# Kernel tuning notes

Hardware: AMD Instinct MI355X
Metric: run time of the kernel (lower is better)

Reference implementation:

```python
import jax, jax.numpy as jnp
import numpy as np

# ---- static configuration (from init_kwargs) ----
K = 2                 # kernel_size -> (2K+1)^2 = 25 window offsets
WIN = 2 * K + 1       # 5
A = WIN * WIN         # 25 window slots (ir_in replicated A times)
MUL_IN = 16           # multiplicity of each input irrep (16x0e + 16x1e)
MUL_OUT = 32          # 32x0e + 32x1e
SH0 = float(1.0 / (2.0 * np.sqrt(np.pi)))       # Y_l=0, e3nn 'integral' norm
SH1 = float(np.sqrt(3.0 / (4.0 * np.pi)))       # Y_l=1 scale (normalize=False)
CG_110 = float(1.0 / np.sqrt(3.0))              # CG for 1x1 -> 0 (dot/sqrt3)
CG_111 = float(1.0 / np.sqrt(2.0))              # CG for 1x1 -> 1 (cross/sqrt2)
# path normalization: out irrep gets 1/sqrt(fan_in) with fan = n_paths * mul_u
A0 = float(1.0 / np.sqrt(2 * A * MUL_IN))       # 0e fed by paths (0e,0e)+(1e,1e) per slot
A1 = float(1.0 / np.sqrt(3 * A * MUL_IN))       # 1e fed by (0e,1e)+(1e,0e)+(1e,1e)


def setup_inputs() -> dict:
    key = jax.random.key(0)
    ks = jax.random.split(key, 7)
    feat = jax.random.normal(ks[0], (8, 64, 64, 64), dtype=jnp.float32)
    spin = jax.random.normal(ks[1], (8, 64, 64, 3), dtype=jnp.float32)
    wshape = (A, MUL_IN, MUL_OUT)  # one uvw block per window slot per path type
    W_000 = jax.random.normal(ks[2], wshape, dtype=jnp.float32)
    W_110 = jax.random.normal(ks[3], wshape, dtype=jnp.float32)
    W_011 = jax.random.normal(ks[4], wshape, dtype=jnp.float32)
    W_101 = jax.random.normal(ks[5], wshape, dtype=jnp.float32)
    W_111 = jax.random.normal(ks[6], wshape, dtype=jnp.float32)
    return {"feat": feat, "spin": spin, "W_000": W_000, "W_110": W_110,
            "W_011": W_011, "W_101": W_101, "W_111": W_111}


def spin2colsq2d(feat):
    # circular im2col: (N,Lx,Ly,F) -> (N,Lx,Ly,A,F)
    N, Lx, Ly, F = feat.shape
    p = jnp.pad(feat, ((0, 0), (K, K), (K, K), (0, 0)), mode='wrap')
    cols = [p[:, ix:ix + Lx, iy:iy + Ly, :]
            for ix in range(WIN) for iy in range(WIN)]
    return jnp.stack(cols, axis=3)


def reference(feat, spin, W_000, W_110, W_011, W_101, W_111):
    col = spin2colsq2d(feat)                                  # (N,Lx,Ly,A,64)
    x0 = col[..., :MUL_IN]                                    # (N,Lx,Ly,A,16) scalars
    x1 = col[..., MUL_IN:].reshape(col.shape[:-1] + (MUL_IN, 3))  # (N,Lx,Ly,A,16,3)
    # spherical harmonics of spin, l=0..1, normalize=False, integral norm
    sh1 = SH1 * spin                                          # (N,Lx,Ly,3)
    # ---- paths into 0e output ----
    dot = jnp.einsum('nxyaui,nxyi->nxyau', x1, sh1) * CG_110  # 1e x 1e -> 0e
    out0 = A0 * (SH0 * jnp.einsum('nxyau,auw->nxyw', x0, W_000)
                 + jnp.einsum('nxyau,auw->nxyw', dot, W_110))  # (N,Lx,Ly,32)
    # ---- paths into 1e output ----
    cross = jnp.cross(x1, sh1[..., None, None, :]) * CG_111   # 1e x 1e -> 1e
    out1 = A1 * (jnp.einsum('nxyau,nxyi,auw->nxywi', x0, sh1, W_011)
                 + SH0 * jnp.einsum('nxyaui,auw->nxywi', x1, W_101)
                 + jnp.einsum('nxyaui,auw->nxywi', cross, W_111))  # (N,Lx,Ly,32,3)
    out1 = out1.reshape(out1.shape[:-2] + (MUL_OUT * 3,))
    return jnp.concatenate([out0, out1], axis=-1)             # (N,Lx,Ly,128)
```

## Files before the change

kernel.cpp:

```cpp
#include <hip/hip_runtime.h>


typedef __attribute__((ext_vector_type(8))) short short8;
typedef __attribute__((ext_vector_type(16))) float f32x16;
typedef __attribute__((ext_vector_type(4))) float float4v;

typedef __attribute__((address_space(3))) unsigned char lds_u8_t;
typedef const __attribute__((address_space(1))) unsigned char g_u8_t;

#define FEATT_BYTES (8u * 64u * 64u * 64u * 2u)
#define BT_OFFSET   FEATT_BYTES

#define MFMA32(A, B, C) __builtin_amdgcn_mfma_f32_32x32x16_bf16(A, B, C, 0, 0, 0)

__device__ __forceinline__ unsigned short f2bf(float f) {
    unsigned int u = __float_as_uint(f);
    return (unsigned short)((u + 0x7FFFu + ((u >> 16) & 1u)) >> 16);
}

__global__ __launch_bounds__(256) void prep_kernel(
    const float* __restrict__ feat,
    const float* __restrict__ W000, const float* __restrict__ W110,
    const float* __restrict__ W011, const float* __restrict__ W101,
    const float* __restrict__ W111,
    unsigned char* __restrict__ ws)
{
    int tid = threadIdx.x;
    int b = blockIdx.x;
    if (b < 512) {
        __shared__ float sf[64][68];
        size_t base = (size_t)b * 4096;
        #pragma unroll
        for (int i = 0; i < 4; ++i) {
            int e = tid + i * 256;
            float4v v = *(const float4v*)(feat + base + (size_t)e * 4);
            int px = e >> 4;
            int c  = (e & 15) * 4;
            sf[px][c + 0] = v[0]; sf[px][c + 1] = v[1];
            sf[px][c + 2] = v[2]; sf[px][c + 3] = v[3];
        }
        __syncthreads();
        unsigned short* dst = (unsigned short*)ws + base;
        #pragma unroll
        for (int i = 0; i < 2; ++i) {
            int t = tid + i * 256;
            int s = t >> 6, px = t & 63;
            short8 o;
            #pragma unroll
            for (int j = 0; j < 8; ++j) {
                int chp = s * 8 + j;
                int c = (chp < 16) ? chp : (16 + 3 * ((chp - 16) & 15) + ((chp - 16) >> 4));
                o[j] = (short)f2bf(sf[px][c]);
            }
            *(short8*)(dst + s * 512 + px * 8) = o;
        }
    } else {
        int t = (b - 512) * 256 + tid;
        if (t >= 4000) return;
        int a = t / 160, colv = t - a * 160;
        int arr = colv >> 5, w = colv & 31;
        const float* Wp = (arr == 0) ? W000 : (arr == 1) ? W011
                        : (arr == 2) ? W110 : (arr == 3) ? W101 : W111;
        unsigned short tmp[16];
        #pragma unroll
        for (int k = 0; k < 16; ++k) tmp[k] = f2bf(Wp[a * 512 + k * 32 + w]);
        unsigned short* d = (unsigned short*)(ws + BT_OFFSET) + (size_t)t * 16;
        *(short8*)(d)     = *(short8*)(tmp);
        *(short8*)(d + 8) = *(short8*)(tmp + 8);
    }
}

__global__ __launch_bounds__(256, 4) void spinconv_mfma_kernel(
    const unsigned char* __restrict__ featT8,
    const unsigned char* __restrict__ bt,
    const float* __restrict__ spin,
    float* __restrict__ out)
{
    const float SH0f   = 0.28209479177387814f;
    const float CG110f = 0.5773502691896258f;
    const float CG111f = 0.7071067811865476f;
    const float A0f    = 0.035355339059327376f;
    const float A1f    = 0.028867513459481287f;

    __shared__ __align__(16) unsigned char fl[1440 * 16];
    __shared__ float s_lds[96];

    int tid = threadIdx.x;
    int b = blockIdx.x;
    int L = ((b & 7) << 7) + (b >> 3);
    int column = L >> 1;
    int x = column & 63;
    int y0 = (L & 1) << 5;

    int lane = tid & 63;
    int wv4 = tid >> 6;

    #pragma unroll
    for (int i = 0; i < 6; ++i) {
        int e = tid + (i << 8);
        int g = e / 36;
        int l = e - g * 36;
        int dx = g >> 3, slot = g & 7;
        int X = (x + dx + 62) & 63;
        int y = (y0 + l + 62) & 63;
        const unsigned char* src = featT8
            + (size_t)(column - x + X) * 8192 + slot * 1024 + y * 16;
        if (e < 1440)
            __builtin_amdgcn_global_load_lds((g_u8_t*)src,
                (lds_u8_t*)(fl + ((i << 8) + (tid & ~63)) * 16), 16, 0, 0);
    }
    if (tid < 96) {
        s_lds[tid] = 0.4886025119029199f
                   * spin[((size_t)column * 64 + y0) * 3 + tid];
    }
    __syncthreads();

    int role = (wv4 + (b & 3)) & 3;
    int col = lane & 31;
    int khalf = lane >> 5;

    const unsigned char* bbase = bt + col * 32 + khalf * 16;
    float* rowbuf = (float*)fl;

    f32x16 zz;
    #pragma unroll
    for (int i = 0; i < 16; ++i) zz[i] = 0.f;

    f32x16 ac0 = zz, ac1 = zz, ac2 = zz;

    if (role == 0) {
        short8 B0c, B1c, B0n, B1n, Axc, Axn;
        auto loadB = [&](int a, short8& b0, short8& b1) {
            const unsigned char* p = bbase + a * 5120;
            b0 = *(const short8*)(p);
            b1 = *(const short8*)(p + 1024);
        };
        auto loadA = [&](int a, short8& ax) {
            int ix = a / 5;
            int iy = a - ix * 5;
            ax = *(const short8*)(fl + ix * 4608 + khalf * 576 + (col + iy) * 16);
        };
        loadB(0, B0c, B1c);
        loadA(0, Axc);
        #pragma unroll
        for (int ap = 0; ap < 25; ap += 2) {
            if (ap + 1 < 25) { loadB(ap + 1, B0n, B1n); loadA(ap + 1, Axn); }
            __builtin_amdgcn_s_setprio(1);
            ac0 = MFMA32(Axc, B0c, ac0);
            ac1 = MFMA32(Axc, B1c, ac1);
            __builtin_amdgcn_s_setprio(0);
            if (ap + 1 < 25) {
                if (ap + 2 < 25) { loadB(ap + 2, B0c, B1c); loadA(ap + 2, Axc); }
                __builtin_amdgcn_s_setprio(1);
                ac0 = MFMA32(Axn, B0n, ac0);
                ac1 = MFMA32(Axn, B1n, ac1);
                __builtin_amdgcn_s_setprio(0);
            }
        }
    } else {
        const int matoff = (role + 1) << 10;
        short8 Bc, Bn, C0c, C1c, C2c, C0n, C1n, C2n;
        auto loadB = [&](int a, short8& bb) {
            bb = *(const short8*)(bbase + a * 5120 + matoff);
        };
        auto loadA = [&](int a, short8& c0, short8& c1, short8& c2) {
            int ix = a / 5;
            int iy = a - ix * 5;
            const unsigned char* ab = fl + ix * 4608 + (col + iy) * 16;
            c0 = *(const short8*)(ab + (2 + khalf) * 576);
            c1 = *(const short8*)(ab + (4 + khalf) * 576);
            c2 = *(const short8*)(ab + (6 + khalf) * 576);
        };
        loadB(0, Bc);
        loadA(0, C0c, C1c, C2c);
        #pragma unroll
        for (int ap = 0; ap < 25; ap += 2) {
            if (ap + 1 < 25) { loadB(ap + 1, Bn); loadA(ap + 1, C0n, C1n, C2n); }
            __builtin_amdgcn_s_setprio(1);
            ac0 = MFMA32(C0c, Bc, ac0);
            ac1 = MFMA32(C1c, Bc, ac1);
            ac2 = MFMA32(C2c, Bc, ac2);
            __builtin_amdgcn_s_setprio(0);
            if (ap + 1 < 25) {
                if (ap + 2 < 25) { loadB(ap + 2, Bc); loadA(ap + 2, C0c, C1c, C2c); }
                __builtin_amdgcn_s_setprio(1);
                ac0 = MFMA32(C0n, Bn, ac0);
                ac1 = MFMA32(C1n, Bn, ac1);
                ac2 = MFMA32(C2n, Bn, ac2);
                __builtin_amdgcn_s_setprio(0);
            }
        }
    }

    __syncthreads();

    {
        if (role == 0) {
            #pragma unroll
            for (int r = 0; r < 16; ++r) {
                int yl = (r & 3) + ((r >> 2) << 3) + (khalf << 2);
                float s0 = s_lds[yl * 3 + 0];
                float s1 = s_lds[yl * 3 + 1];
                float s2 = s_lds[yl * 3 + 2];
                float S000 = ac0[r], S011 = ac1[r];
                float* rb = rowbuf + yl * 128;
                float* rp = rb + 32 + 3 * col;
                rb[col] = A0f * SH0f * S000;
                rp[0] = A1f * s0 * S011;
                rp[1] = A1f * s1 * S011;
                rp[2] = A1f * s2 * S011;
            }
        }
        __syncthreads();
        if (role == 1) {
            #pragma unroll
            for (int r = 0; r < 16; ++r) {
                int yl = (r & 3) + ((r >> 2) << 3) + (khalf << 2);
                float s0 = s_lds[yl * 3 + 0];
                float s1 = s_lds[yl * 3 + 1];
                float s2 = s_lds[yl * 3 + 2];
                rowbuf[yl * 128 + col] +=
                    A0f * CG110f * (s0 * ac0[r] + s1 * ac1[r] + s2 * ac2[r]);
            }
        } else if (role == 2) {
            #pragma unroll
            for (int r = 0; r < 16; ++r) {
                int yl = (r & 3) + ((r >> 2) << 3) + (khalf << 2);
                float* rp = rowbuf + yl * 128 + 32 + 3 * col;
                rp[0] += A1f * SH0f * ac0[r];
                rp[1] += A1f * SH0f * ac1[r];
                rp[2] += A1f * SH0f * ac2[r];
            }
        }
        __syncthreads();
        if (role == 3) {
            #pragma unroll
            for (int r = 0; r < 16; ++r) {
                int yl = (r & 3) + ((r >> 2) << 3) + (khalf << 2);
                float s0 = s_lds[yl * 3 + 0];
                float s1 = s_lds[yl * 3 + 1];
                float s2 = s_lds[yl * 3 + 2];
                float U0 = ac0[r], U1 = ac1[r], U2 = ac2[r];
                float* rp = rowbuf + yl * 128 + 32 + 3 * col;
                rp[0] += A1f * CG111f * (U1 * s2 - U2 * s1);
                rp[1] += A1f * CG111f * (U2 * s0 - U0 * s2);
                rp[2] += A1f * CG111f * (U0 * s1 - U1 * s0);
            }
        }
        __syncthreads();
    }

    float* ob = out + ((size_t)column * 64 + y0) * 128;
    #pragma unroll
    for (int i = 0; i < 4; ++i) {
        int e = (tid + (i << 8)) << 2;
        *(float4v*)(ob + e) = *(const float4v*)(rowbuf + e);
    }
}

extern "C" void kernel_launch(void* const* d_in, const int* in_sizes, int n_in,
                              void* d_out, int out_size, void* d_ws, size_t ws_size,
                              hipStream_t stream) {
    const float* feat = (const float*)d_in[0];
    const float* spin = (const float*)d_in[1];
    const float* W000 = (const float*)d_in[2];
    const float* W110 = (const float*)d_in[3];
    const float* W011 = (const float*)d_in[4];
    const float* W101 = (const float*)d_in[5];
    const float* W111 = (const float*)d_in[6];
    float* out = (float*)d_out;
    unsigned char* ws = (unsigned char*)d_ws;

    hipLaunchKernelGGL(prep_kernel, dim3(528), dim3(256), 0, stream,
                       feat, W000, W110, W011, W101, W111, ws);
    hipLaunchKernelGGL(spinconv_mfma_kernel, dim3(1024), dim3(256), 0, stream,
                       ws, ws + BT_OFFSET, spin, out);
}
```

Baseline: 24.60 us.

## Process two half-columns per block with double-buffered LDS prefetch

Each block now handles a full 64-row column as two 32-row halves. It issues the global-to-LDS loads for both halves up front and waits only on the first half (vmcnt(5)) before starting the first half's MFMAs, so the second half's load overlaps compute. The grid is halved to 512 blocks, LDS use roughly doubles, and the occupancy hint drops from 4 to 3 blocks per CU. The cost is fewer resident blocks and reliance on a hand-set waitcnt matching exactly how many loads each thread issued.

```diff
diff --git a/kernel.cpp b/kernel.cpp
--- a/kernel.cpp
+++ b/kernel.cpp
@@ -70,7 +70,7 @@
     }
 }
 
-__global__ __launch_bounds__(256, 4) void spinconv_mfma_kernel(
+__global__ __launch_bounds__(256, 3) void spinconv_mfma_kernel(
     const unsigned char* __restrict__ featT8,
     const unsigned char* __restrict__ bt,
     const float* __restrict__ spin,
@@ -82,126 +82,134 @@
     const float A0f    = 0.035355339059327376f;
     const float A1f    = 0.028867513459481287f;
 
-    __shared__ __align__(16) unsigned char fl[1440 * 16];
-    __shared__ float s_lds[96];
+    __shared__ __align__(16) unsigned char fl[2][23040];
+    __shared__ float s_lds[192];
 
     int tid = threadIdx.x;
     int b = blockIdx.x;
-    int L = ((b & 7) << 7) + (b >> 3);
-    int column = L >> 1;
+    int column = ((b & 7) << 6) + (b >> 3);
     int x = column & 63;
-    int y0 = (L & 1) << 5;
+    int colbase = column - x;
 
     int lane = tid & 63;
     int wv4 = tid >> 6;
 
+    float spinval = 0.f;
+    if (tid < 192) spinval = 0.4886025119029199f * spin[(size_t)column * 192 + tid];
+
     #pragma unroll
-    for (int i = 0; i < 6; ++i) {
-        int e = tid + (i << 8);
-        int g = e / 36;
-        int l = e - g * 36;
-        int dx = g >> 3, slot = g & 7;
-        int X = (x + dx + 62) & 63;
-        int y = (y0 + l + 62) & 63;
-        const unsigned char* src = featT8
-            + (size_t)(column - x + X) * 8192 + slot * 1024 + y * 16;
-        if (e < 1440)
-            __builtin_amdgcn_global_load_lds((g_u8_t*)src,
-                (lds_u8_t*)(fl + ((i << 8) + (tid & ~63)) * 16), 16, 0, 0);
+    for (int th = 0; th < 2; ++th) {
+        #pragma unroll
+        for (int i = 0; i < 6; ++i) {
+            int e = tid + (i << 8);
+            if (e < 1440) {
+                int g = e / 36;
+                int l = e - g * 36;
+                int dx = g >> 3, slot = g & 7;
+                int X = (x + dx + 62) & 63;
+                int y = ((th << 5) + l + 62) & 63;
+                const unsigned char* src = featT8
+                    + (size_t)(colbase + X) * 8192 + slot * 1024 + y * 16;
+                __builtin_amdgcn_global_load_lds((g_u8_t*)src,
+                    (lds_u8_t*)(fl[th] + ((i << 8) + (tid & ~63)) * 16), 16, 0, 0);
+            }
+        }
     }
-    if (tid < 96) {
-        s_lds[tid] = 0.4886025119029199f
-                   * spin[((size_t)column * 64 + y0) * 3 + tid];
-    }
-    __syncthreads();
+    asm volatile("s_waitcnt vmcnt(5)" ::: "memory");
+    __builtin_amdgcn_sched_barrier(0);
+    __builtin_amdgcn_s_barrier();
 
     int role = (wv4 + (b & 3)) & 3;
     int col = lane & 31;
     int khalf = lane >> 5;
-
     const unsigned char* bbase = bt + col * 32 + khalf * 16;
-    float* rowbuf = (float*)fl;
 
     f32x16 zz;
     #pragma unroll
     for (int i = 0; i < 16; ++i) zz[i] = 0.f;
 
-    f32x16 ac0 = zz, ac1 = zz, ac2 = zz;
-
-    if (role == 0) {
-        short8 B0c, B1c, B0n, B1n, Axc, Axn;
-        auto loadB = [&](int a, short8& b0, short8& b1) {
-            const unsigned char* p = bbase + a * 5120;
-            b0 = *(const short8*)(p);
-            b1 = *(const short8*)(p + 1024);
-        };
-        auto loadA = [&](int a, short8& ax) {
-            int ix = a / 5;
-            int iy = a - ix * 5;
-            ax = *(const short8*)(fl + ix * 4608 + khalf * 576 + (col + iy) * 16);
-        };
-        loadB(0, B0c, B1c);
-        loadA(0, Axc);
-        #pragma unroll
-        for (int ap = 0; ap < 25; ap += 2) {
-            if (ap + 1 < 25) { loadB(ap + 1, B0n, B1n); loadA(ap + 1, Axn); }
-            __builtin_amdgcn_s_setprio(1);
-            ac0 = MFMA32(Axc, B0c, ac0);
-            ac1 = MFMA32(Axc, B1c, ac1);
-            __builtin_amdgcn_s_setprio(0);
-            if (ap + 1 < 25) {
-                if (ap + 2 < 25) { loadB(ap + 2, B0c, B1c); loadA(ap + 2, Axc); }
+    #pragma unroll
+    for (int th = 0; th < 2; ++th) {
+        const unsigned char* ft = fl[th];
+        f32x16 ac0 = zz, ac1 = zz, ac2 = zz;
+
+        if (role == 0) {
+            short8 B0c, B1c, B0n, B1n, Axc, Axn;
+            auto loadB = [&](int a, short8& b0, short8& b1) {
+                const unsigned char* p = bbase + a * 5120;
+                b0 = *(const short8*)(p);
+                b1 = *(const short8*)(p + 1024);
+            };
+            auto loadA = [&](int a, short8& ax) {
+                int ix = a / 5;
+                int iy = a - ix * 5;
+                ax = *(const short8*)(ft + ix * 4608 + khalf * 576 + (col + iy) * 16);
+            };
+            loadB(0, B0c, B1c);
+            loadA(0, Axc);
+            #pragma unroll
+            for (int ap = 0; ap < 25; ap += 2) {
+                if (ap + 1 < 25) { loadB(ap + 1, B0n, B1n); loadA(ap + 1, Axn); }
                 __builtin_amdgcn_s_setprio(1);
-                ac0 = MFMA32(Axn, B0n, ac0);
-                ac1 = MFMA32(Axn, B1n, ac1);
+                ac0 = MFMA32(Axc, B0c, ac0);
+                ac1 = MFMA32(Axc, B1c, ac1);
                 __builtin_amdgcn_s_setprio(0);
-            }
-        }
-    } else {
-        const int matoff = (role + 1) << 10;
-        short8 Bc, Bn, C0c, C1c, C2c, C0n, C1n, C2n;
-        auto loadB = [&](int a, short8& bb) {
-            bb = *(const short8*)(bbase + a * 5120 + matoff);
-        };
-        auto loadA = [&](int a, short8& c0, short8& c1, short8& c2) {
-            int ix = a / 5;
-            int iy = a - ix * 5;
-            const unsigned char* ab = fl + ix * 4608 + (col + iy) * 16;
-            c0 = *(const short8*)(ab + (2 + khalf) * 576);
-            c1 = *(const short8*)(ab + (4 + khalf) * 576);
-            c2 = *(const short8*)(ab + (6 + khalf) * 576);
-        };
-        loadB(0, Bc);
-        loadA(0, C0c, C1c, C2c);
-        #pragma unroll
-        for (int ap = 0; ap < 25; ap += 2) {
-            if (ap + 1 < 25) { loadB(ap + 1, Bn); loadA(ap + 1, C0n, C1n, C2n); }
-            __builtin_amdgcn_s_setprio(1);
-            ac0 = MFMA32(C0c, Bc, ac0);
-            ac1 = MFMA32(C1c, Bc, ac1);
-            ac2 = MFMA32(C2c, Bc, ac2);
-            __builtin_amdgcn_s_setprio(0);
-            if (ap + 1 < 25) {
-                if (ap + 2 < 25) { loadB(ap + 2, Bc); loadA(ap + 2, C0c, C1c, C2c); }
+                if (ap + 1 < 25) {
+                    if (ap + 2 < 25) { loadB(ap + 2, B0c, B1c); loadA(ap + 2, Axc); }
+                    __builtin_amdgcn_s_setprio(1);
+                    ac0 = MFMA32(Axn, B0n, ac0);
+                    ac1 = MFMA32(Axn, B1n, ac1);
+                    __builtin_amdgcn_s_setprio(0);
+                }
+            }
+        } else {
+            const int matoff = (role + 1) << 10;
+            short8 Bc, Bn, C0c, C1c, C2c, C0n, C1n, C2n;
+            auto loadB = [&](int a, short8& bb) {
+                bb = *(const short8*)(bbase + a * 5120 + matoff);
+            };
+            auto loadA = [&](int a, short8& c0, short8& c1, short8& c2) {
+                int ix = a / 5;
+                int iy = a - ix * 5;
+                const unsigned char* ab = ft + ix * 4608 + (col + iy) * 16;
+                c0 = *(const short8*)(ab + (2 + khalf) * 576);
+                c1 = *(const short8*)(ab + (4 + khalf) * 576);
+                c2 = *(const short8*)(ab + (6 + khalf) * 576);
+            };
+            loadB(0, Bc);
+            loadA(0, C0c, C1c, C2c);
+            #pragma unroll
+            for (int ap = 0; ap < 25; ap += 2) {
+                if (ap + 1 < 25) { loadB(ap + 1, Bn); loadA(ap + 1, C0n, C1n, C2n); }
                 __builtin_amdgcn_s_setprio(1);
-                ac0 = MFMA32(C0n, Bn, ac0);
-                ac1 = MFMA32(C1n, Bn, ac1);
-                ac2 = MFMA32(C2n, Bn, ac2);
+                ac0 = MFMA32(C0c, Bc, ac0);
+                ac1 = MFMA32(C1c, Bc, ac1);
+                ac2 = MFMA32(C2c, Bc, ac2);
                 __builtin_amdgcn_s_setprio(0);
-            }
-        }
-    }
-
-    __syncthreads();
-
-    {
+                if (ap + 1 < 25) {
+                    if (ap + 2 < 25) { loadB(ap + 2, Bc); loadA(ap + 2, C0c, C1c, C2c); }
+                    __builtin_amdgcn_s_setprio(1);
+                    ac0 = MFMA32(C0n, Bn, ac0);
+                    ac1 = MFMA32(C1n, Bn, ac1);
+                    ac2 = MFMA32(C2n, Bn, ac2);
+                    __builtin_amdgcn_s_setprio(0);
+                }
+            }
+        }
+
+        if (th == 0 && tid < 192) s_lds[tid] = spinval;
+        __syncthreads();
+
+        float* rowbuf = (float*)fl[th];
+        const float* sp = s_lds + th * 96;
+
         if (role == 0) {
             #pragma unroll
             for (int r = 0; r < 16; ++r) {
                 int yl = (r & 3) + ((r >> 2) << 3) + (khalf << 2);
-                float s0 = s_lds[yl * 3 + 0];
-                float s1 = s_lds[yl * 3 + 1];
-                float s2 = s_lds[yl * 3 + 2];
+                float s0 = sp[yl * 3 + 0];
+                float s1 = sp[yl * 3 + 1];
+                float s2 = sp[yl * 3 + 2];
                 float S000 = ac0[r], S011 = ac1[r];
                 float* rb = rowbuf + yl * 128;
                 float* rp = rb + 32 + 3 * col;
@@ -216,9 +224,9 @@
             #pragma unroll
             for (int r = 0; r < 16; ++r) {
                 int yl = (r & 3) + ((r >> 2) << 3) + (khalf << 2);
-                float s0 = s_lds[yl * 3 + 0];
-                float s1 = s_lds[yl * 3 + 1];
-                float s2 = s_lds[yl * 3 + 2];
+                float s0 = sp[yl * 3 + 0];
+                float s1 = sp[yl * 3 + 1];
+                float s2 = sp[yl * 3 + 2];
                 rowbuf[yl * 128 + col] +=
                     A0f * CG110f * (s0 * ac0[r] + s1 * ac1[r] + s2 * ac2[r]);
             }
@@ -237,9 +245,9 @@
             #pragma unroll
             for (int r = 0; r < 16; ++r) {
                 int yl = (r & 3) + ((r >> 2) << 3) + (khalf << 2);
-                float s0 = s_lds[yl * 3 + 0];
-                float s1 = s_lds[yl * 3 + 1];
-                float s2 = s_lds[yl * 3 + 2];
+                float s0 = sp[yl * 3 + 0];
+                float s1 = sp[yl * 3 + 1];
+                float s2 = sp[yl * 3 + 2];
                 float U0 = ac0[r], U1 = ac1[r], U2 = ac2[r];
                 float* rp = rowbuf + yl * 128 + 32 + 3 * col;
                 rp[0] += A1f * CG111f * (U1 * s2 - U2 * s1);
@@ -248,13 +256,13 @@
             }
         }
         __syncthreads();
-    }
-
-    float* ob = out + ((size_t)column * 64 + y0) * 128;
-    #pragma unroll
-    for (int i = 0; i < 4; ++i) {
-        int e = (tid + (i << 8)) << 2;
-        *(float4v*)(ob + e) = *(const float4v*)(rowbuf + e);
+
+        float* ob = out + ((size_t)column * 64 + (th << 5)) * 128;
+        #pragma unroll
+        for (int i = 0; i < 4; ++i) {
+            int e = (tid + (i << 8)) << 2;
+            *(float4v*)(ob + e) = *(const float4v*)(rowbuf + e);
+        }
     }
 }
 
@@ -273,6 +281,6 @@
 
     hipLaunchKernelGGL(prep_kernel, dim3(528), dim3(256), 0, stream,
                        feat, W000, W110, W011, W101, W111, ws);
-    hipLaunchKernelGGL(spinconv_mfma_kernel, dim3(1024), dim3(256), 0, stream,
+    hipLaunchKernelGGL(spinconv_mfma_kernel, dim3(512), dim3(256), 0, stream,
                        ws, ws + BT_OFFSET, spin, out);
 }
```

New measurement: 26.65 us. 8.3% more time.

## Split work across two waves per block and write outputs directly from registers

Applied to the files above, without the earlier changes.

Reduces the block from four waves to two. Wave 0 computes the 0e-output paths plus the scalar-to-vector path, and wave 1 computes the W101 and W111 vector paths with six accumulators. The LDS rowbuf staging and its multiple barrier-separated accumulate phases are replaced by a small LDS exchange of one accumulator, followed by direct global stores of the combined results. This removes the serialized epilogue and most barriers. In exchange each wave issues more MFMAs and holds more live registers, so there are fewer waves per block to hide latency, and the scattered 12-byte stores are less coalesced.

```diff
diff --git a/kernel.cpp b/kernel.cpp
--- a/kernel.cpp
+++ b/kernel.cpp
@@ -12,6 +12,8 @@
 #define BT_OFFSET   FEATT_BYTES
 
 #define MFMA32(A, B, C) __builtin_amdgcn_mfma_f32_32x32x16_bf16(A, B, C, 0, 0, 0)
+
+struct F3 { float a, b, c; };
 
 __device__ __forceinline__ unsigned short f2bf(float f) {
     unsigned int u = __float_as_uint(f);
@@ -70,7 +72,7 @@
     }
 }
 
-__global__ __launch_bounds__(256, 4) void spinconv_mfma_kernel(
+__global__ __launch_bounds__(128, 3) void spinconv_mfma_kernel(
     const unsigned char* __restrict__ featT8,
     const unsigned char* __restrict__ bt,
     const float* __restrict__ spin,
@@ -83,6 +85,7 @@
     const float A1f    = 0.028867513459481287f;
 
     __shared__ __align__(16) unsigned char fl[1440 * 16];
+    __shared__ float sbuf[16][64];
     __shared__ float s_lds[96];
 
     int tid = threadIdx.x;
@@ -93,21 +96,22 @@
     int y0 = (L & 1) << 5;
 
     int lane = tid & 63;
-    int wv4 = tid >> 6;
+    int wv = tid >> 6;
 
     #pragma unroll
-    for (int i = 0; i < 6; ++i) {
-        int e = tid + (i << 8);
-        int g = e / 36;
-        int l = e - g * 36;
-        int dx = g >> 3, slot = g & 7;
-        int X = (x + dx + 62) & 63;
-        int y = (y0 + l + 62) & 63;
-        const unsigned char* src = featT8
-            + (size_t)(column - x + X) * 8192 + slot * 1024 + y * 16;
-        if (e < 1440)
+    for (int i = 0; i < 12; ++i) {
+        int e = tid + (i << 7);
+        if (e < 1440) {
+            int g = e / 36;
+            int l = e - g * 36;
+            int dx = g >> 3, slot = g & 7;
+            int X = (x + dx + 62) & 63;
+            int y = (y0 + l + 62) & 63;
+            const unsigned char* src = featT8
+                + (size_t)(column - x + X) * 8192 + slot * 1024 + y * 16;
             __builtin_amdgcn_global_load_lds((g_u8_t*)src,
-                (lds_u8_t*)(fl + ((i << 8) + (tid & ~63)) * 16), 16, 0, 0);
+                (lds_u8_t*)(fl + ((i << 7) + (tid & ~63)) * 16), 16, 0, 0);
+        }
     }
     if (tid < 96) {
         s_lds[tid] = 0.4886025119029199f
@@ -115,53 +119,67 @@
     }
     __syncthreads();
 
-    int role = (wv4 + (b & 3)) & 3;
+    int role = wv ^ (b & 1);
     int col = lane & 31;
     int khalf = lane >> 5;
-
     const unsigned char* bbase = bt + col * 32 + khalf * 16;
-    float* rowbuf = (float*)fl;
 
     f32x16 zz;
     #pragma unroll
     for (int i = 0; i < 16; ++i) zz[i] = 0.f;
 
-    f32x16 ac0 = zz, ac1 = zz, ac2 = zz;
+    f32x16 ac0 = zz, ac1 = zz, ac2 = zz, ac3 = zz, ac4 = zz, ac5 = zz;
 
     if (role == 0) {
-        short8 B0c, B1c, B0n, B1n, Axc, Axn;
-        auto loadB = [&](int a, short8& b0, short8& b1) {
+        short8 B0c, B1c, B2c, B0n, B1n, B2n;
+        short8 Axc, C0c, C1c, C2c, Axn, C0n, C1n, C2n;
+        auto loadB = [&](int a, short8& b0, short8& b1, short8& b2) {
             const unsigned char* p = bbase + a * 5120;
             b0 = *(const short8*)(p);
             b1 = *(const short8*)(p + 1024);
-        };
-        auto loadA = [&](int a, short8& ax) {
+            b2 = *(const short8*)(p + 2048);
+        };
+        auto loadA = [&](int a, short8& ax, short8& c0, short8& c1, short8& c2) {
             int ix = a / 5;
             int iy = a - ix * 5;
-            ax = *(const short8*)(fl + ix * 4608 + khalf * 576 + (col + iy) * 16);
-        };
-        loadB(0, B0c, B1c);
-        loadA(0, Axc);
+            const unsigned char* ab = fl + ix * 4608 + (col + iy) * 16;
+            ax = *(const short8*)(ab + khalf * 576);
+            c0 = *(const short8*)(ab + (2 + khalf) * 576);
+            c1 = *(const short8*)(ab + (4 + khalf) * 576);
+            c2 = *(const short8*)(ab + (6 + khalf) * 576);
+        };
+        loadB(0, B0c, B1c, B2c);
+        loadA(0, Axc, C0c, C1c, C2c);
         #pragma unroll
         for (int ap = 0; ap < 25; ap += 2) {
-            if (ap + 1 < 25) { loadB(ap + 1, B0n, B1n); loadA(ap + 1, Axn); }
+            if (ap + 1 < 25) { loadB(ap + 1, B0n, B1n, B2n); loadA(ap + 1, Axn, C0n, C1n, C2n); }
             __builtin_amdgcn_s_setprio(1);
             ac0 = MFMA32(Axc, B0c, ac0);
             ac1 = MFMA32(Axc, B1c, ac1);
+            ac2 = MFMA32(C0c, B2c, ac2);
+            ac3 = MFMA32(C1c, B2c, ac3);
+            ac4 = MFMA32(C2c, B2c, ac4);
             __builtin_amdgcn_s_setprio(0);
             if (ap + 1 < 25) {
-                if (ap + 2 < 25) { loadB(ap + 2, B0c, B1c); loadA(ap + 2, Axc); }
+                if (ap + 2 < 25) { loadB(ap + 2, B0c, B1c, B2c); loadA(ap + 2, Axc, C0c, C1c, C2c); }
                 __builtin_amdgcn_s_setprio(1);
                 ac0 = MFMA32(Axn, B0n, ac0);
                 ac1 = MFMA32(Axn, B1n, ac1);
+                ac2 = MFMA32(C0n, B2n, ac2);
+                ac3 = MFMA32(C1n, B2n, ac3);
+                ac4 = MFMA32(C2n, B2n, ac4);
                 __builtin_amdgcn_s_setprio(0);
             }
         }
+        #pragma unroll
+        for (int r = 0; r < 16; ++r) sbuf[r][lane] = ac1[r];
     } else {
-        const int matoff = (role + 1) << 10;
-        short8 Bc, Bn, C0c, C1c, C2c, C0n, C1n, C2n;
-        auto loadB = [&](int a, short8& bb) {
-            bb = *(const short8*)(bbase + a * 5120 + matoff);
+        short8 B3c, B4c, B3n, B4n;
+        short8 C0c, C1c, C2c, C0n, C1n, C2n;
+        auto loadB = [&](int a, short8& b3, short8& b4) {
+            const unsigned char* p = bbase + a * 5120;
+            b3 = *(const short8*)(p + 3072);
+            b4 = *(const short8*)(p + 4096);
         };
         auto loadA = [&](int a, short8& c0, short8& c1, short8& c2) {
             int ix = a / 5;
@@ -171,22 +189,28 @@
             c1 = *(const short8*)(ab + (4 + khalf) * 576);
             c2 = *(const short8*)(ab + (6 + khalf) * 576);
         };
-        loadB(0, Bc);
+        loadB(0, B3c, B4c);
         loadA(0, C0c, C1c, C2c);
         #pragma unroll
         for (int ap = 0; ap < 25; ap += 2) {
-            if (ap + 1 < 25) { loadB(ap + 1, Bn); loadA(ap + 1, C0n, C1n, C2n); }
+            if (ap + 1 < 25) { loadB(ap + 1, B3n, B4n); loadA(ap + 1, C0n, C1n, C2n); }
             __builtin_amdgcn_s_setprio(1);
-            ac0 = MFMA32(C0c, Bc, ac0);
-            ac1 = MFMA32(C1c, Bc, ac1);
-            ac2 = MFMA32(C2c, Bc, ac2);
+            ac0 = MFMA32(C0c, B3c, ac0);
+            ac3 = MFMA32(C0c, B4c, ac3);
+            ac1 = MFMA32(C1c, B3c, ac1);
+            ac4 = MFMA32(C1c, B4c, ac4);
+            ac2 = MFMA32(C2c, B3c, ac2);
+            ac5 = MFMA32(C2c, B4c, ac5);
             __builtin_amdgcn_s_setprio(0);
             if (ap + 1 < 25) {
-                if (ap + 2 < 25) { loadB(ap + 2, Bc); loadA(ap + 2, C0c, C1c, C2c); }
+                if (ap + 2 < 25) { loadB(ap + 2, B3c, B4c); loadA(ap + 2, C0c, C1c, C2c); }
                 __builtin_amdgcn_s_setprio(1);
-                ac0 = MFMA32(C0n, Bn, ac0);
-                ac1 = MFMA32(C1n, Bn, ac1);
-                ac2 = MFMA32(C2n, Bn, ac2);
+                ac0 = MFMA32(C0n, B3n, ac0);
+                ac3 = MFMA32(C0n, B4n, ac3);
+                ac1 = MFMA32(C1n, B3n, ac1);
+                ac4 = MFMA32(C1n, B4n, ac4);
+                ac2 = MFMA32(C2n, B3n, ac2);
+                ac5 = MFMA32(C2n, B4n, ac5);
                 __builtin_amdgcn_s_setprio(0);
             }
         }
@@ -194,67 +218,34 @@
 
     __syncthreads();
 
-    {
-        if (role == 0) {
-            #pragma unroll
-            for (int r = 0; r < 16; ++r) {
-                int yl = (r & 3) + ((r >> 2) << 3) + (khalf << 2);
-                float s0 = s_lds[yl * 3 + 0];
-                float s1 = s_lds[yl * 3 + 1];
-                float s2 = s_lds[yl * 3 + 2];
-                float S000 = ac0[r], S011 = ac1[r];
-                float* rb = rowbuf + yl * 128;
-                float* rp = rb + 32 + 3 * col;
-                rb[col] = A0f * SH0f * S000;
-                rp[0] = A1f * s0 * S011;
-                rp[1] = A1f * s1 * S011;
-                rp[2] = A1f * s2 * S011;
-            }
-        }
-        __syncthreads();
-        if (role == 1) {
-            #pragma unroll
-            for (int r = 0; r < 16; ++r) {
-                int yl = (r & 3) + ((r >> 2) << 3) + (khalf << 2);
-                float s0 = s_lds[yl * 3 + 0];
-                float s1 = s_lds[yl * 3 + 1];
-                float s2 = s_lds[yl * 3 + 2];
-                rowbuf[yl * 128 + col] +=
-                    A0f * CG110f * (s0 * ac0[r] + s1 * ac1[r] + s2 * ac2[r]);
-            }
-        } else if (role == 2) {
-            #pragma unroll
-            for (int r = 0; r < 16; ++r) {
-                int yl = (r & 3) + ((r >> 2) << 3) + (khalf << 2);
-                float* rp = rowbuf + yl * 128 + 32 + 3 * col;
-                rp[0] += A1f * SH0f * ac0[r];
-                rp[1] += A1f * SH0f * ac1[r];
-                rp[2] += A1f * SH0f * ac2[r];
-            }
-        }
-        __syncthreads();
-        if (role == 3) {
-            #pragma unroll
-            for (int r = 0; r < 16; ++r) {
-                int yl = (r & 3) + ((r >> 2) << 3) + (khalf << 2);
-                float s0 = s_lds[yl * 3 + 0];
-                float s1 = s_lds[yl * 3 + 1];
-                float s2 = s_lds[yl * 3 + 2];
-                float U0 = ac0[r], U1 = ac1[r], U2 = ac2[r];
-                float* rp = rowbuf + yl * 128 + 32 + 3 * col;
-                rp[0] += A1f * CG111f * (U1 * s2 - U2 * s1);
-                rp[1] += A1f * CG111f * (U2 * s0 - U0 * s2);
-                rp[2] += A1f * CG111f * (U0 * s1 - U1 * s0);
-            }
-        }
-        __syncthreads();
-    }
-
-    float* ob = out + ((size_t)column * 64 + y0) * 128;
-    #pragma unroll
-    for (int i = 0; i < 4; ++i) {
-        int e = (tid + (i << 8)) << 2;
-        *(float4v*)(ob + e) = *(const float4v*)(rowbuf + e);
+    size_t pbase = (size_t)column * 64 + y0;
+    if (role == 0) {
+        #pragma unroll
+        for (int r = 0; r < 16; ++r) {
+            int pxin = (r & 3) + ((r >> 2) << 3) + (khalf << 2);
+            float s0 = s_lds[pxin * 3 + 0];
+            float s1 = s_lds[pxin * 3 + 1];
+            float s2 = s_lds[pxin * 3 + 2];
+            float o0 = A0f * (SH0f * ac0[r]
+                     + CG110f * (s0 * ac2[r] + s1 * ac3[r] + s2 * ac4[r]));
+            out[(pbase + pxin) * 128 + col] = o0;
+        }
+    } else {
+        #pragma unroll
+        for (int r = 0; r < 16; ++r) {
+            int pxin = (r & 3) + ((r >> 2) << 3) + (khalf << 2);
+            float s0 = s_lds[pxin * 3 + 0];
+            float s1 = s_lds[pxin * 3 + 1];
+            float s2 = s_lds[pxin * 3 + 2];
+            float S011 = sbuf[r][lane];
+            float T0 = ac0[r], T1 = ac1[r], T2 = ac2[r];
+            float U0 = ac3[r], U1 = ac4[r], U2 = ac5[r];
+            F3 v;
+            v.a = A1f * (s0 * S011 + SH0f * T0 + CG111f * (U1 * s2 - U2 * s1));
+            v.b = A1f * (s1 * S011 + SH0f * T1 + CG111f * (U2 * s0 - U0 * s2));
+            v.c = A1f * (s2 * S011 + SH0f * T2 + CG111f * (U0 * s1 - U1 * s0));
+            *(F3*)(out + (pbase + pxin) * 128 + 32 + 3 * col) = v;
+        }
     }
 }
 
@@ -273,6 +264,6 @@
 
     hipLaunchKernelGGL(prep_kernel, dim3(528), dim3(256), 0, stream,
                        feat, W000, W110, W011, W101, W111, ws);
-    hipLaunchKernelGGL(spinconv_mfma_kernel, dim3(1024), dim3(256), 0, stream,
+    hipLaunchKernelGGL(spinconv_mfma_kernel, dim3(1024), dim3(128), 0, stream,
                        ws, ws + BT_OFFSET, spin, out);
 }
```

Measured after the change: 22.84 us. 7.1% less time.
